# Kernel optimization log

Measured on AMD Instinct MI355X. Metric: run time of the kernel, lower is better.

The kernel has to match this reference:

```python
import jax, jax.numpy as jnp
import numpy as np
import math

NUM_HEADS = 16
ROPE_BASE = 10000.0


def apply_rope(t):
    # t: [B, H, S, D] with D even. Interleaved-pair rotary embedding (torchtune-style).
    D = t.shape[-1]
    S = t.shape[-2]
    inv_freq = 1.0 / (ROPE_BASE ** (jnp.arange(0, D, 2, dtype=jnp.float32) / D))  # [D/2]
    angles = jnp.arange(S, dtype=jnp.float32)[:, None] * inv_freq[None, :]  # [S, D/2]
    cos = jnp.cos(angles).astype(t.dtype)  # [S, D/2]
    sin = jnp.sin(angles).astype(t.dtype)
    t1 = t[..., 0::2]  # [B, H, S, D/2]
    t2 = t[..., 1::2]
    r1 = t1 * cos - t2 * sin
    r2 = t1 * sin + t2 * cos
    # interleave back
    out = jnp.stack([r1, r2], axis=-1).reshape(t.shape)
    return out


def setup_inputs() -> dict:
    key = jax.random.key(0)
    ks = jax.random.split(key, 6)
    B, S, D = 4, 2048, 2048
    s_in = 1.0 / math.sqrt(D)
    x = jax.random.normal(ks[0], (B, S, D), dtype=jnp.float32)
    wq = jax.random.normal(ks[1], (D, D), dtype=jnp.float32) * s_in
    wk = jax.random.normal(ks[2], (D, D), dtype=jnp.float32) * s_in
    wv = jax.random.normal(ks[3], (D, D), dtype=jnp.float32) * s_in
    wo = jax.random.normal(ks[4], (D, D), dtype=jnp.float32) * s_in
    bo = jnp.zeros((D,), dtype=jnp.float32)
    return {"x": x, "wq": wq, "wk": wk, "wv": wv, "wo": wo, "bo": bo}


def reference(x, wq, wk, wv, wo, bo):
    B, S, D = x.shape
    H = NUM_HEADS
    hd = D // H
    # QKV projections (nn.Linear: y = x @ W^T)
    q = (x @ wq.T).reshape(B, S, H, hd).transpose(0, 2, 1, 3)  # [B,H,S,hd]
    k = (x @ wk.T).reshape(B, S, H, hd).transpose(0, 2, 1, 3)
    v = (x @ wv.T).reshape(B, S, H, hd).transpose(0, 2, 1, 3)
    q = apply_rope(q)
    k = apply_rope(k)
    # causal SDPA (dropout_p = 0 in eval)
    scale = 1.0 / math.sqrt(hd)
    scores = jnp.einsum('bhqd,bhkd->bhqk', q, k) * scale  # [B,H,S,S]
    causal = jnp.tril(jnp.ones((S, S), dtype=bool))
    scores = jnp.where(causal, scores, jnp.finfo(scores.dtype).min)
    attn = jax.nn.softmax(scores, axis=-1)
    ctx = jnp.einsum('bhqk,bhkd->bqhd', attn, v).reshape(B, S, D)
    return ctx @ wo.T + bo
```

## Files before the change

### kernel.cpp

```cpp
#include <hip/hip_runtime.h>

typedef short short8 __attribute__((ext_vector_type(8)));
typedef float f32x4 __attribute__((ext_vector_type(4)));
typedef unsigned int u32x4 __attribute__((ext_vector_type(4)));
typedef unsigned short u16x4 __attribute__((ext_vector_type(4)));
typedef unsigned short u16x8 __attribute__((ext_vector_type(8)));

__device__ __forceinline__ unsigned short f2bf(float f) {
  unsigned int u = __builtin_bit_cast(unsigned int, f);
  u += 0x7fffu + ((u >> 16) & 1u);
  return (unsigned short)(u >> 16);
}
__device__ __forceinline__ float bf2f(unsigned short h) {
  unsigned int u = ((unsigned int)h) << 16;
  return __builtin_bit_cast(float, u);
}

__device__ __forceinline__ void gl16(const unsigned short* g, unsigned short* l) {
  __builtin_amdgcn_global_load_lds((const __attribute__((address_space(1))) unsigned int*)g,
                                   (__attribute__((address_space(3))) unsigned int*)l, 16, 0, 0);
}

#define BB 4
#define SS 2048
#define DD 2048
#define HH 16
#define HD 128
#define MM (BB * SS)

__global__ void cast_all(const float* __restrict__ x, const float* __restrict__ wq,
                         const float* __restrict__ wk, const float* __restrict__ wv,
                         const float* __restrict__ wo, unsigned short* __restrict__ xb,
                         unsigned short* __restrict__ wqb, unsigned short* __restrict__ wkb,
                         unsigned short* __restrict__ wvb, unsigned short* __restrict__ wob) {
  int i = blockIdx.x * blockDim.x + threadIdx.x;
  const int X4 = (MM * DD) / 4;
  const int W4 = (DD * DD) / 4;
  const float* src;
  unsigned short* dst;
  int off;
  if (i < X4) {
    src = x; dst = xb; off = i;
  } else {
    int t = i - X4;
    int w = t >> 20;
    off = t & (W4 - 1);
    src = (w == 0) ? wq : (w == 1) ? wk : (w == 2) ? wv : wo;
    dst = (w == 0) ? wqb : (w == 1) ? wkb : (w == 2) ? wvb : wob;
  }
  f32x4 v = ((const f32x4*)src)[off];
  u16x4 o;
  o[0] = f2bf(v[0]); o[1] = f2bf(v[1]); o[2] = f2bf(v[2]); o[3] = f2bf(v[3]);
  ((u16x4*)dst)[off] = o;
}

#define STGH(P, R0, t, h, moff)                                                     \
  do {                                                                              \
    const unsigned short* _s =                                                      \
        (P) + (size_t)((R0) + (h) * 128 + srow) * DD + (size_t)((t) * 64 + scol);   \
    gl16(_s, lds + (moff) + (h) * 8192 + wvi * 512);                                \
    gl16(_s + (size_t)64 * DD, lds + (moff) + (h) * 8192 + 4096 + wvi * 512);       \
  } while (0)

#define BARRIER asm volatile("s_barrier" ::: "memory")

__device__ __forceinline__ void gemm_core(const unsigned short* __restrict__ Ap,
                                          const unsigned short* __restrict__ Bp,
                                          unsigned short* lds, int rt, int ct,
                                          f32x4 (&acc)[8][4]) {
  const int tid = threadIdx.x;
  const int lane = tid & 63, wvi = tid >> 6;
  const int wm = wvi >> 2, wn = wvi & 3;
  const int quad = lane >> 4, l16 = lane & 15;
  const int srow = wvi * 8 + (lane >> 3);
  const int scol = ((lane & 7) ^ (lane >> 3)) << 3;
  const int ck0 = (quad ^ (l16 & 7)) << 3;
  const int ck1 = ((4 + quad) ^ (l16 & 7)) << 3;
  const int aro = (wm * 128 + l16) << 6;
  const int bro = (wn * 64 + l16) << 6;
  const int rb = rt * 256, cb = ct * 256;

#pragma unroll
  for (int i = 0; i < 8; ++i)
#pragma unroll
    for (int j = 0; j < 4; ++j) acc[i][j] = f32x4{0.f, 0.f, 0.f, 0.f};

  STGH(Bp, cb, 0, 0, 16384);
  STGH(Bp, cb, 0, 1, 16384);
  STGH(Ap, rb, 0, 0, 0);
  STGH(Ap, rb, 0, 1, 0);
  STGH(Bp, cb, 1, 0, 49152);
  STGH(Bp, cb, 1, 1, 49152);
  asm volatile("s_waitcnt vmcnt(4)" ::: "memory");
  BARRIER;

#pragma unroll 2
  for (int t = 0; t < 32; ++t) {
    const unsigned short* ab = lds + ((t & 1) << 15);
    const unsigned short* bb = ab + 16384;
    const int pn = ((t + 1) & 1) << 15;
    const int pc = ((t & 1) << 15) + 16384;
    short8 aq[4][2], b0f[2][2], b1f[2][2];

#pragma unroll
    for (int mi = 0; mi < 4; ++mi) {
      aq[mi][0] = __builtin_bit_cast(short8, *(const u32x4*)(ab + aro + mi * 1024 + ck0));
      aq[mi][1] = __builtin_bit_cast(short8, *(const u32x4*)(ab + aro + mi * 1024 + ck1));
    }
#pragma unroll
    for (int ni = 0; ni < 2; ++ni) {
      b0f[ni][0] = __builtin_bit_cast(short8, *(const u32x4*)(bb + bro + ni * 1024 + ck0));
      b0f[ni][1] = __builtin_bit_cast(short8, *(const u32x4*)(bb + bro + ni * 1024 + ck1));
    }
    if (t < 31) STGH(Ap, rb, t + 1, 0, pn);
    BARRIER;
    __builtin_amdgcn_s_setprio(1);
#pragma unroll
    for (int k = 0; k < 2; ++k)
#pragma unroll
      for (int mi = 0; mi < 4; ++mi)
#pragma unroll
        for (int ni = 0; ni < 2; ++ni)
          acc[mi][ni] =
              __builtin_amdgcn_mfma_f32_16x16x32_bf16(aq[mi][k], b0f[ni][k], acc[mi][ni], 0, 0, 0);
    __builtin_amdgcn_s_setprio(0);
    BARRIER;

#pragma unroll
    for (int ni = 0; ni < 2; ++ni) {
      b1f[ni][0] = __builtin_bit_cast(short8, *(const u32x4*)(bb + bro + 2048 + ni * 1024 + ck0));
      b1f[ni][1] = __builtin_bit_cast(short8, *(const u32x4*)(bb + bro + 2048 + ni * 1024 + ck1));
    }
    if (t < 31) STGH(Ap, rb, t + 1, 1, pn);
    BARRIER;
    __builtin_amdgcn_s_setprio(1);
#pragma unroll
    for (int k = 0; k < 2; ++k)
#pragma unroll
      for (int mi = 0; mi < 4; ++mi)
#pragma unroll
        for (int ni = 0; ni < 2; ++ni)
          acc[mi][2 + ni] = __builtin_amdgcn_mfma_f32_16x16x32_bf16(aq[mi][k], b1f[ni][k],
                                                                    acc[mi][2 + ni], 0, 0, 0);
    __builtin_amdgcn_s_setprio(0);
    BARRIER;

#pragma unroll
    for (int mi = 0; mi < 4; ++mi) {
      aq[mi][0] = __builtin_bit_cast(short8, *(const u32x4*)(ab + aro + 4096 + mi * 1024 + ck0));
      aq[mi][1] = __builtin_bit_cast(short8, *(const u32x4*)(ab + aro + 4096 + mi * 1024 + ck1));
    }
    if (t < 30) STGH(Bp, cb, t + 2, 0, pc);
    BARRIER;
    __builtin_amdgcn_s_setprio(1);
#pragma unroll
    for (int k = 0; k < 2; ++k)
#pragma unroll
      for (int mi = 0; mi < 4; ++mi)
#pragma unroll
        for (int ni = 0; ni < 2; ++ni)
          acc[4 + mi][2 + ni] = __builtin_amdgcn_mfma_f32_16x16x32_bf16(
              aq[mi][k], b1f[ni][k], acc[4 + mi][2 + ni], 0, 0, 0);
    __builtin_amdgcn_s_setprio(0);
    BARRIER;

    if (t < 30) STGH(Bp, cb, t + 2, 1, pc);
    BARRIER;
    __builtin_amdgcn_s_setprio(1);
#pragma unroll
    for (int k = 0; k < 2; ++k)
#pragma unroll
      for (int mi = 0; mi < 4; ++mi)
#pragma unroll
        for (int ni = 0; ni < 2; ++ni)
          acc[4 + mi][ni] = __builtin_amdgcn_mfma_f32_16x16x32_bf16(aq[mi][k], b0f[ni][k],
                                                                    acc[4 + mi][ni], 0, 0, 0);
    __builtin_amdgcn_s_setprio(0);
    if (t < 30) {
      asm volatile("s_waitcnt vmcnt(4)" ::: "memory");
      BARRIER;
    } else if (t == 30) {
      asm volatile("s_waitcnt vmcnt(0)" ::: "memory");
      BARRIER;
    }
  }
}

__global__ __launch_bounds__(512, 2) void gemm_qkv(const unsigned short* __restrict__ A,
                                                   const unsigned short* __restrict__ W0,
                                                   const unsigned short* __restrict__ W1,
                                                   const unsigned short* __restrict__ W2,
                                                   unsigned short* __restrict__ q_out,
                                                   unsigned short* __restrict__ k_out,
                                                   unsigned short* __restrict__ v_out) {
  __shared__ unsigned short lds[65536];
  const int ct = blockIdx.x, rt = blockIdx.y, z = blockIdx.z;
  const unsigned short* W = (z == 0) ? W0 : (z == 1) ? W1 : W2;
  unsigned short* outb = (z == 0) ? q_out : (z == 1) ? k_out : v_out;
  f32x4 acc[8][4];
  gemm_core(A, W, lds, rt, ct, acc);

  const int tid = threadIdx.x;
  const int lane = tid & 63, wvi = tid >> 6;
  const int wm = wvi >> 2, wn = wvi & 3;
  const int quad = lane >> 4, l16 = lane & 15;
#pragma unroll
  for (int mi = 0; mi < 8; ++mi)
#pragma unroll
    for (int ni = 0; ni < 4; ++ni)
#pragma unroll
      for (int r = 0; r < 4; ++r) {
        int row_g = rt * 256 + wm * 128 + mi * 16 + quad * 4 + r;
        int col_g = ct * 256 + wn * 64 + ni * 16 + l16;
        float v = acc[mi][ni][r];
        int b = row_g >> 11, s = row_g & (SS - 1);
        int h = col_g >> 7, d = col_g & (HD - 1);
        size_t rowbase = (((size_t)(b * HH + h)) * SS + (size_t)s) * HD;
        if (z == 1) {
          outb[rowbase + (size_t)((((d >> 3) ^ (s & 7)) << 3) | (d & 7))] = f2bf(v);
        } else {
          outb[rowbase + (size_t)d] = f2bf(v);
        }
      }
}

__global__ __launch_bounds__(512, 2) void gemm_out(const unsigned short* __restrict__ A,
                                                   const unsigned short* __restrict__ W,
                                                   float* __restrict__ outf,
                                                   const float* __restrict__ bias) {
  __shared__ unsigned short lds[65536];
  const int ct = blockIdx.x, rt = blockIdx.y;
  f32x4 acc[8][4];
  gemm_core(A, W, lds, rt, ct, acc);

  const int tid = threadIdx.x;
  const int lane = tid & 63, wvi = tid >> 6;
  const int wm = wvi >> 2, wn = wvi & 3;
  const int quad = lane >> 4, l16 = lane & 15;
#pragma unroll
  for (int mi = 0; mi < 8; ++mi)
#pragma unroll
    for (int ni = 0; ni < 4; ++ni)
#pragma unroll
      for (int r = 0; r < 4; ++r) {
        int row_g = rt * 256 + wm * 128 + mi * 16 + quad * 4 + r;
        int col_g = ct * 256 + wn * 64 + ni * 16 + l16;
        outf[(size_t)row_g * DD + col_g] = acc[mi][ni][r] + bias[col_g];
      }
}

__global__ void rope_kernel(unsigned short* __restrict__ qb, unsigned short* __restrict__ kb) {
  int id = blockIdx.x * blockDim.x + threadIdx.x;
  int c = id & 15;
  int s = (id >> 4) & (SS - 1);
  int bhb = id >> 15;
  unsigned short* p;
  float psc;
  if (bhb < 64) {
    p = qb + ((size_t)bhb * SS + s) * HD + c * 8;
    psc = 0.08838834764831845f;
  } else {
    p = kb + ((size_t)(bhb & 63) * SS + s) * HD + ((c ^ (s & 7)) << 3);
    psc = 1.0f;
  }
  u32x4 w = *(u32x4*)p;
  const float nl = -9.210340371976184f / 64.0f;
  u32x4 o;
#pragma unroll
  for (int j = 0; j < 4; ++j) {
    int pi = c * 4 + j;
    float inv = __expf((float)pi * nl);
    float ang = (float)s * inv;
    float cs = __cosf(ang), sn = __sinf(ang);
    float e = bf2f((unsigned short)(w[j] & 0xffffu));
    float od = bf2f((unsigned short)(w[j] >> 16));
    float r1 = (e * cs - od * sn) * psc;
    float r2 = (e * sn + od * cs) * psc;
    o[j] = (unsigned int)f2bf(r1) | ((unsigned int)f2bf(r2) << 16);
  }
  *(u32x4*)p = o;
}

__global__ __launch_bounds__(512, 2) void attn_kernel(const unsigned short* __restrict__ qb,
                                                      const unsigned short* __restrict__ kb,
                                                      const unsigned short* __restrict__ vb,
                                                      unsigned short* __restrict__ ctxb) {
  __shared__ unsigned short lds[40960];
  const int tid = threadIdx.x;
  const int g0 = blockIdx.x;
  const int g = (g0 & 7) * 128 + (g0 >> 3);
  const int bh = g >> 4;
  const int qa = 15 - (g & 15);
  const int lane = tid & 63, wvi = tid >> 6;
  const int quad = lane >> 4, l16 = lane & 15;
  const size_t bhq = (size_t)bh * SS * HD;
  const int qrow = qa * 128 + wvi * 16;
  const int b = bh >> 4, h = bh & (HH - 1);
  unsigned short* Pw = lds + 32768 + wvi * 1024;
  const int vrr = tid & 31, vcd = tid >> 5;
  const int krow = wvi * 4 + (lane >> 4);
  const int kcol = (lane & 15) * 8;
  f32x4 zero = {0.f, 0.f, 0.f, 0.f};

  short8 qf[4];
#pragma unroll
  for (int ks = 0; ks < 4; ++ks)
    qf[ks] = __builtin_bit_cast(
        short8, *(const u32x4*)(qb + bhq + (size_t)(qrow + l16) * HD + ks * 32 + quad * 8));

  f32x4 acc[8];
#pragma unroll
  for (int dt = 0; dt < 8; ++dt) acc[dt] = zero;
  float lpart[4] = {0.f, 0.f, 0.f, 0.f};

  const int ntile = 2 * qa + 2;

  {
    const unsigned short* vsrc = vb + bhq + (size_t)(2 * vrr) * HD + vcd * 8;
    u32x4 pva = *(const u32x4*)vsrc;
    u32x4 pvb = *(const u32x4*)(vsrc + HD);
    gl16(kb + bhq + (size_t)krow * HD + kcol, lds + krow * 128);
    gl16(kb + bhq + (size_t)(32 + krow) * HD + kcol, lds + (32 + krow) * 128);
    u16x8 va = __builtin_bit_cast(u16x8, pva);
    u16x8 vb2 = __builtin_bit_cast(u16x8, pvb);
    unsigned int* vw = (unsigned int*)(lds + 16384);
#pragma unroll
    for (int j = 0; j < 8; ++j)
      vw[(vcd * 8 + j) * 32 + (((vrr >> 2) ^ j) << 2) + (vrr & 3)] =
          (unsigned int)va[j] | ((unsigned int)vb2[j] << 16);
    __syncthreads();
  }

  for (int kt = 0; kt < ntile; ++kt) {
    const int kv0 = kt * 64;
    const int cur = (kt & 1) * 8192;
    const int nxt = ((kt + 1) & 1) * 8192;
    const unsigned short* Kc = lds + cur;
    const unsigned short* Vc = lds + 16384 + cur;
    const bool hasnext = (kt + 1 < ntile);

    u32x4 pva, pvb;
    if (hasnext) {
      const int kvn = kv0 + 64;
      const unsigned short* vsrc = vb + bhq + (size_t)(kvn + 2 * vrr) * HD + vcd * 8;
      pva = *(const u32x4*)vsrc;
      pvb = *(const u32x4*)(vsrc + HD);
      gl16(kb + bhq + (size_t)(kvn + krow) * HD + kcol, lds + nxt + krow * 128);
      gl16(kb + bhq + (size_t)(kvn + 32 + krow) * HD + kcol, lds + nxt + (32 + krow) * 128);
    }

    f32x4 sc[4];
#pragma unroll
    for (int nt = 0; nt < 4; ++nt) {
      sc[nt] = zero;
#pragma unroll
      for (int ks = 0; ks < 4; ++ks) {
        short8 kf = __builtin_bit_cast(
            short8, *(const u32x4*)(Kc + (nt * 16 + l16) * 128 +
                                    (((ks * 4 + quad) ^ (l16 & 7)) << 3)));
        sc[nt] = __builtin_amdgcn_mfma_f32_16x16x32_bf16(qf[ks], kf, sc[nt], 0, 0, 0);
      }
    }

    const bool dm = (kt >= ntile - 2);
    if (dm) {
#pragma unroll
      for (int r = 0; r < 4; ++r) {
        int row = qrow + quad * 4 + r;
        int prow = quad * 4 + r;
#pragma unroll
        for (int nt = 0; nt < 4; ++nt) {
          int col = kv0 + nt * 16 + l16;
          float pv = (col > row) ? 0.f : __expf(sc[nt][r]);
          lpart[r] += pv;
          int el = prow * 64 +
                   ((((nt * 2 + (l16 >> 3)) + prow + 4 * (prow >> 3)) & 7) << 3) + (l16 & 7);
          Pw[el] = f2bf(pv);
        }
      }
    } else {
#pragma unroll
      for (int r = 0; r < 4; ++r) {
        int prow = quad * 4 + r;
#pragma unroll
        for (int nt = 0; nt < 4; ++nt) {
          float pv = __expf(sc[nt][r]);
          lpart[r] += pv;
          int el = prow * 64 +
                   ((((nt * 2 + (l16 >> 3)) + prow + 4 * (prow >> 3)) & 7) << 3) + (l16 & 7);
          Pw[el] = f2bf(pv);
        }
      }
    }

#pragma unroll
    for (int ks2 = 0; ks2 < 2; ++ks2) {
      short8 pfrag = __builtin_bit_cast(
          short8, *(const u32x4*)(Pw + l16 * 64 +
                                  ((((ks2 * 4 + quad) + l16 + 4 * (l16 >> 3)) & 7) << 3)));
#pragma unroll
      for (int dt = 0; dt < 8; ++dt) {
        short8 vf = __builtin_bit_cast(
            short8, *(const u32x4*)(Vc + (dt * 16 + l16) * 64 +
                                    (((ks2 * 4 + quad) ^ (l16 & 7)) << 3)));
        acc[dt] = __builtin_amdgcn_mfma_f32_16x16x32_bf16(pfrag, vf, acc[dt], 0, 0, 0);
      }
    }

    if (hasnext) {
      u16x8 va = __builtin_bit_cast(u16x8, pva);
      u16x8 vb2 = __builtin_bit_cast(u16x8, pvb);
      unsigned int* vw = (unsigned int*)(lds + 16384 + nxt);
#pragma unroll
      for (int j = 0; j < 8; ++j)
        vw[(vcd * 8 + j) * 32 + (((vrr >> 2) ^ j) << 2) + (vrr & 3)] =
            (unsigned int)va[j] | ((unsigned int)vb2[j] << 16);
    }
    __syncthreads();
  }

  float rl[4];
#pragma unroll
  for (int r = 0; r < 4; ++r) {
    float rs = lpart[r];
#pragma unroll
    for (int off = 1; off < 16; off <<= 1) rs += __shfl_xor(rs, off, 64);
    rl[r] = 1.0f / rs;
  }
#pragma unroll
  for (int dt = 0; dt < 8; ++dt)
#pragma unroll
    for (int r = 0; r < 4; ++r) {
      int row = qrow + quad * 4 + r;
      ctxb[((size_t)(b * SS + row)) * DD + h * HD + dt * 16 + l16] = f2bf(acc[dt][r] * rl[r]);
    }
}

extern "C" void kernel_launch(void* const* d_in, const int* in_sizes, int n_in,
                              void* d_out, int out_size, void* d_ws, size_t ws_size,
                              hipStream_t stream) {
  const float* x = (const float*)d_in[0];
  const float* wq = (const float*)d_in[1];
  const float* wk = (const float*)d_in[2];
  const float* wv = (const float*)d_in[3];
  const float* wo = (const float*)d_in[4];
  const float* bo = (const float*)d_in[5];
  float* out = (float*)d_out;

  unsigned short* xb = (unsigned short*)d_ws;
  unsigned short* wqb = xb + (size_t)MM * DD;
  unsigned short* wkb = wqb + (size_t)DD * DD;
  unsigned short* wvb = wkb + (size_t)DD * DD;
  unsigned short* wob = wvb + (size_t)DD * DD;
  unsigned short* qb = wob + (size_t)DD * DD;
  unsigned short* kb = qb + (size_t)MM * DD;
  unsigned short* vb = kb + (size_t)MM * DD;
  unsigned short* ctxb = vb + (size_t)MM * DD;

  cast_all<<<(2 * MM * DD / 4) / 256, 256, 0, stream>>>(x, wq, wk, wv, wo, xb, wqb, wkb, wvb, wob);

  dim3 gg(DD / 256, MM / 256, 3);
  gemm_qkv<<<gg, 512, 0, stream>>>(xb, wqb, wkb, wvb, qb, kb, vb);

  rope_kernel<<<(128 * 2048 * 16) / 256, 256, 0, stream>>>(qb, kb);

  attn_kernel<<<1024, 512, 0, stream>>>(qb, kb, vb, ctxb);

  dim3 go(DD / 256, MM / 256);
  gemm_out<<<go, 512, 0, stream>>>(ctxb, wob, out, bo);
}
```

Before: 572.6 us.

## Fuse RoPE into QKV GEMM epilogue and remap GEMM block order

Removes the standalone RoPE kernel and applies the rotary rotation and the Q scaling inside the QKV GEMM epilogue. Each lane fetches its interleaved partner value with a lane shuffle and computes cos/sin per element. The change also remaps block indices in both GEMMs so that consecutive blocks are spread across column tiles, which is meant to improve L2 reuse across XCDs. This saves one read-modify-write pass over Q and K, at the cost of extra transcendental math in the epilogue, where the rotation is applied to fp32 accumulators instead of bf16-rounded values.

```diff
diff --git a/kernel.cpp b/kernel.cpp
--- a/kernel.cpp
+++ b/kernel.cpp
@@ -194,7 +194,10 @@
                                                    unsigned short* __restrict__ k_out,
                                                    unsigned short* __restrict__ v_out) {
   __shared__ unsigned short lds[65536];
-  const int ct = blockIdx.x, rt = blockIdx.y, z = blockIdx.z;
+  const int id = (blockIdx.z << 8) | (blockIdx.y << 3) | blockIdx.x;
+  const int nid = (id & 7) * 96 + (id >> 3);
+  const int z = nid >> 8;
+  const int rt = (nid & 255) >> 3, ct = nid & 7;
   const unsigned short* W = (z == 0) ? W0 : (z == 1) ? W1 : W2;
   unsigned short* outb = (z == 0) ? q_out : (z == 1) ? k_out : v_out;
   f32x4 acc[8][4];
@@ -204,24 +207,51 @@
   const int lane = tid & 63, wvi = tid >> 6;
   const int wm = wvi >> 2, wn = wvi & 3;
   const int quad = lane >> 4, l16 = lane & 15;
-#pragma unroll
-  for (int mi = 0; mi < 8; ++mi)
+
+  if (z == 2) {
+#pragma unroll
+    for (int mi = 0; mi < 8; ++mi)
+#pragma unroll
+      for (int ni = 0; ni < 4; ++ni)
+#pragma unroll
+        for (int r = 0; r < 4; ++r) {
+          int row_g = rt * 256 + wm * 128 + mi * 16 + quad * 4 + r;
+          int col_g = ct * 256 + wn * 64 + ni * 16 + l16;
+          int b = row_g >> 11, s = row_g & (SS - 1);
+          int h = col_g >> 7, d = col_g & (HD - 1);
+          outb[(((size_t)(b * HH + h)) * SS + (size_t)s) * HD + (size_t)d] = f2bf(acc[mi][ni][r]);
+        }
+  } else {
+    const float psc = (z == 0) ? 0.08838834764831845f : 1.0f;
+    const bool odd = (l16 & 1) != 0;
+    const float nl = -0.14391156831212936f;
+    float inv4[4];
 #pragma unroll
     for (int ni = 0; ni < 4; ++ni)
-#pragma unroll
-      for (int r = 0; r < 4; ++r) {
-        int row_g = rt * 256 + wm * 128 + mi * 16 + quad * 4 + r;
-        int col_g = ct * 256 + wn * 64 + ni * 16 + l16;
-        float v = acc[mi][ni][r];
-        int b = row_g >> 11, s = row_g & (SS - 1);
-        int h = col_g >> 7, d = col_g & (HD - 1);
-        size_t rowbase = (((size_t)(b * HH + h)) * SS + (size_t)s) * HD;
-        if (z == 1) {
-          outb[rowbase + (size_t)((((d >> 3) ^ (s & 7)) << 3) | (d & 7))] = f2bf(v);
-        } else {
-          outb[rowbase + (size_t)d] = f2bf(v);
+      inv4[ni] = __expf((float)((((wn * 64 + ni * 16 + l16) & 127) >> 1)) * nl);
+#pragma unroll
+    for (int mi = 0; mi < 8; ++mi)
+#pragma unroll
+      for (int ni = 0; ni < 4; ++ni)
+#pragma unroll
+        for (int r = 0; r < 4; ++r) {
+          int row_g = rt * 256 + wm * 128 + mi * 16 + quad * 4 + r;
+          int col_g = ct * 256 + wn * 64 + ni * 16 + l16;
+          int b = row_g >> 11, s = row_g & (SS - 1);
+          int h = col_g >> 7, d = col_g & (HD - 1);
+          float v = acc[mi][ni][r];
+          float p = __shfl_xor(v, 1, 64);
+          float ang = (float)s * inv4[ni];
+          float cs = __cosf(ang), sn = __sinf(ang);
+          float o = (odd ? (p * sn + v * cs) : (v * cs - p * sn)) * psc;
+          size_t rowbase = (((size_t)(b * HH + h)) * SS + (size_t)s) * HD;
+          if (z == 1) {
+            outb[rowbase + (size_t)((((d >> 3) ^ (s & 7)) << 3) | (d & 7))] = f2bf(o);
+          } else {
+            outb[rowbase + (size_t)d] = f2bf(o);
+          }
         }
-      }
+  }
 }
 
 __global__ __launch_bounds__(512, 2) void gemm_out(const unsigned short* __restrict__ A,
@@ -229,7 +259,9 @@
                                                    float* __restrict__ outf,
                                                    const float* __restrict__ bias) {
   __shared__ unsigned short lds[65536];
-  const int ct = blockIdx.x, rt = blockIdx.y;
+  const int id = (blockIdx.y << 3) | blockIdx.x;
+  const int nid = (id & 7) * 32 + (id >> 3);
+  const int rt = nid >> 3, ct = nid & 7;
   f32x4 acc[8][4];
   gemm_core(A, W, lds, rt, ct, acc);
 
@@ -247,38 +279,6 @@
         int col_g = ct * 256 + wn * 64 + ni * 16 + l16;
         outf[(size_t)row_g * DD + col_g] = acc[mi][ni][r] + bias[col_g];
       }
-}
-
-__global__ void rope_kernel(unsigned short* __restrict__ qb, unsigned short* __restrict__ kb) {
-  int id = blockIdx.x * blockDim.x + threadIdx.x;
-  int c = id & 15;
-  int s = (id >> 4) & (SS - 1);
-  int bhb = id >> 15;
-  unsigned short* p;
-  float psc;
-  if (bhb < 64) {
-    p = qb + ((size_t)bhb * SS + s) * HD + c * 8;
-    psc = 0.08838834764831845f;
-  } else {
-    p = kb + ((size_t)(bhb & 63) * SS + s) * HD + ((c ^ (s & 7)) << 3);
-    psc = 1.0f;
-  }
-  u32x4 w = *(u32x4*)p;
-  const float nl = -9.210340371976184f / 64.0f;
-  u32x4 o;
-#pragma unroll
-  for (int j = 0; j < 4; ++j) {
-    int pi = c * 4 + j;
-    float inv = __expf((float)pi * nl);
-    float ang = (float)s * inv;
-    float cs = __cosf(ang), sn = __sinf(ang);
-    float e = bf2f((unsigned short)(w[j] & 0xffffu));
-    float od = bf2f((unsigned short)(w[j] >> 16));
-    float r1 = (e * cs - od * sn) * psc;
-    float r2 = (e * sn + od * cs) * psc;
-    o[j] = (unsigned int)f2bf(r1) | ((unsigned int)f2bf(r2) << 16);
-  }
-  *(u32x4*)p = o;
 }
 
 __global__ __launch_bounds__(512, 2) void attn_kernel(const unsigned short* __restrict__ qb,
@@ -462,8 +462,6 @@
   dim3 gg(DD / 256, MM / 256, 3);
   gemm_qkv<<<gg, 512, 0, stream>>>(xb, wqb, wkb, wvb, qb, kb, vb);
 
-  rope_kernel<<<(128 * 2048 * 16) / 256, 256, 0, stream>>>(qb, kb);
-
   attn_kernel<<<1024, 512, 0, stream>>>(qb, kb, vb, ctxb);
 
   dim3 go(DD / 256, MM / 256);
```

Result: faster. 559.2 us (-2.3%).
